# Kernel optimization log

Measured on AMD Instinct MI355X. Metric: run time of the kernel, lower is better.

Reference implementation:

```python
import jax, jax.numpy as jnp
import numpy as np

N = 100000
E = 1600000
IN_DIM = 20
HID = 32
HEADS = 4
OUT = 64
NEG_SLOPE = 0.2


def _p(key, shape, scale=0.1):
    return jax.random.normal(key, shape, dtype=jnp.float32) * scale


def setup_inputs() -> dict:
    key = jax.random.key(0)
    ks = jax.random.split(key, 20)
    x = jax.random.normal(ks[0], (N, IN_DIM), dtype=jnp.float32)
    edge_index = jax.random.randint(ks[1], (2, E), 0, N, dtype=jnp.int32)
    edge_attr = jax.random.uniform(ks[2], (E, 1), dtype=jnp.float32)
    HC1 = HEADS * HID
    return {
        "x": x,
        "edge_index": edge_index,
        "edge_attr": edge_attr,
        "Wl1": _p(ks[3], (HC1, IN_DIM)), "bl1": jnp.zeros((HC1,), jnp.float32),
        "Wr1": _p(ks[4], (HC1, IN_DIM)), "br1": jnp.zeros((HC1,), jnp.float32),
        "We1": _p(ks[5], (HC1, 1)),
        "att1": _p(ks[6], (HEADS, HID)),
        "b1": jnp.zeros((HC1,), jnp.float32),
        "Wl2": _p(ks[7], (OUT, HC1)), "bl2": jnp.zeros((OUT,), jnp.float32),
        "Wr2": _p(ks[8], (OUT, HC1)), "br2": jnp.zeros((OUT,), jnp.float32),
        "We2": _p(ks[9], (OUT, 1)),
        "att2": _p(ks[10], (1, OUT)),
        "b2": jnp.zeros((OUT,), jnp.float32),
    }


def gatv2_conv(x, src, dst, edge_attr, Wl, bl, Wr, br, We, att, bias, heads, ch, concat):
    n = x.shape[0]
    # add self loops; edge_attr fill_value = mean (PyG default)
    loop = jnp.arange(n, dtype=src.dtype)
    src = jnp.concatenate([src, loop])
    dst = jnp.concatenate([dst, loop])
    ea_fill = jnp.broadcast_to(edge_attr.mean(axis=0, keepdims=True), (n, edge_attr.shape[1]))
    edge_attr = jnp.concatenate([edge_attr, ea_fill], axis=0)

    xl = (x @ Wl.T + bl).reshape(n, heads, ch)   # source transform [N,H,C]
    xr = (x @ Wr.T + br).reshape(n, heads, ch)   # target transform [N,H,C]
    ee = (edge_attr @ We.T).reshape(-1, heads, ch)  # edge embed [E',H,C]

    e = xl[src] + xr[dst] + ee                    # [E',H,C]
    e = jax.nn.leaky_relu(e, NEG_SLOPE)
    logits = jnp.einsum('ehc,hc->eh', e, att)     # [E',H]

    # segment softmax over destination nodes (every node has a self loop)
    mx = jax.ops.segment_max(logits, dst, num_segments=n)
    ex = jnp.exp(logits - mx[dst])
    denom = jax.ops.segment_sum(ex, dst, num_segments=n)
    alpha = ex / denom[dst]                       # [E',H]

    msg = xl[src] * alpha[:, :, None]             # [E',H,C]
    out = jax.ops.segment_sum(msg, dst, num_segments=n)  # [N,H,C]
    out = out.reshape(n, heads * ch) if concat else out.mean(axis=1)
    return out + bias


def reference(x, edge_index, edge_attr, Wl1, bl1, Wr1, br1, We1, att1, b1,
              Wl2, bl2, Wr2, br2, We2, att2, b2):
    src, dst = edge_index[0], edge_index[1]
    h = gatv2_conv(x, src, dst, edge_attr, Wl1, bl1, Wr1, br1, We1, att1, b1,
                   HEADS, HID, concat=True)
    h = jax.nn.elu(h)  # dropout is identity in eval mode
    out = gatv2_conv(h, src, dst, edge_attr, Wl2, bl2, Wr2, br2, We2, att2, b2,
                     1, OUT, concat=False)
    return out
```

## Files before the change

### kernel.cpp

```cpp
#include <hip/hip_runtime.h>
#include <cstdint>
#include <cstddef>

#define NNODES 100000
#define NEDGES 1600000
#define IN_DIM 20
#define HID    32
#define HEADS  4
#define HC1    128
#define OUTC   64
#define NEG    0.2f
#define LOG2E  1.4426950408889634f
#define NCHUNK ((NNODES + 255) / 256)
#define NBLK   ((NNODES + 63) / 64)

typedef _Float16 h2 __attribute__((ext_vector_type(2)));
typedef __fp16   hh2 __attribute__((ext_vector_type(2)));
union U4H { uint4 u; h2 h[4]; };
union U2H { uint2 u; h2 h[2]; };

#if __has_builtin(__builtin_amdgcn_fdot2)
#define FDOT2(a, b, c) __builtin_amdgcn_fdot2(__builtin_bit_cast(hh2, (a)), __builtin_bit_cast(hh2, (b)), (c), false)
#else
#define FDOT2(a, b, c) ((c) + (float)(a).x * (float)(b).x + (float)(a).y * (float)(b).y)
#endif

__global__ void k_sum(const float* __restrict__ ea, int n, float* __restrict__ out) {
    float s = 0.0f;
    for (int i = blockIdx.x * blockDim.x + threadIdx.x; i < n; i += gridDim.x * blockDim.x)
        s += ea[i];
    #pragma unroll
    for (int off = 32; off > 0; off >>= 1) s += __shfl_down(s, off, 64);
    __shared__ float ls[4];
    int lane = threadIdx.x & 63, wid = threadIdx.x >> 6;
    if (lane == 0) ls[wid] = s;
    __syncthreads();
    if (threadIdx.x == 0) {
        float t = ls[0] + ls[1] + ls[2] + ls[3];
        atomicAdd(out, t);
    }
}

__global__ void k_hist(const int* __restrict__ ei, int* __restrict__ cnt,
                       int* __restrict__ erank) {
    int e = blockIdx.x * blockDim.x + threadIdx.x;
    if (e < NEDGES) erank[e] = atomicAdd(&cnt[ei[NEDGES + e]], 1);
}

__global__ void k_scan_chunk(const int* __restrict__ cnt, int* __restrict__ rowptr,
                             int* __restrict__ csums) {
    __shared__ int s[256];
    int i = blockIdx.x * 256 + threadIdx.x;
    int v = (i < NNODES) ? cnt[i] : 0;
    s[threadIdx.x] = v;
    __syncthreads();
    for (int off = 1; off < 256; off <<= 1) {
        int t = (threadIdx.x >= off) ? s[threadIdx.x - off] : 0;
        __syncthreads();
        s[threadIdx.x] += t;
        __syncthreads();
    }
    if (i < NNODES) rowptr[i] = s[threadIdx.x] - v;
    if (threadIdx.x == 255) csums[blockIdx.x] = s[255];
}

__global__ void k_scan_tops(int* __restrict__ csums) {
    __shared__ int s[512];
    int v = (threadIdx.x < NCHUNK) ? csums[threadIdx.x] : 0;
    s[threadIdx.x] = v;
    __syncthreads();
    for (int off = 1; off < 512; off <<= 1) {
        int t = (threadIdx.x >= off) ? s[threadIdx.x - off] : 0;
        __syncthreads();
        s[threadIdx.x] += t;
        __syncthreads();
    }
    if (threadIdx.x < NCHUNK) csums[threadIdx.x] = s[threadIdx.x] - v;
}

__global__ void k_scan_add(int* __restrict__ rowptr, const int* __restrict__ csums) {
    int i = blockIdx.x * 256 + threadIdx.x;
    if (i < NNODES) rowptr[i] += csums[blockIdx.x];
    if (i == 0) rowptr[NNODES] = NEDGES;
}

__global__ void k_scatter(const int* __restrict__ ei, const float* __restrict__ ea,
                          const int* __restrict__ rowptr, const int* __restrict__ erank,
                          int2* __restrict__ cedge) {
    int e = blockIdx.x * blockDim.x + threadIdx.x;
    if (e >= NEDGES) return;
    int dst = ei[NEDGES + e];
    int pos = rowptr[dst] + erank[e];
    cedge[pos] = make_int2(ei[e], __float_as_int(ea[e]));
}

__global__ void k_prep(const float* __restrict__ Wl1, const float* __restrict__ Wr1,
                       float* __restrict__ Bt1,
                       const float* __restrict__ Wl2, const float* __restrict__ Wr2,
                       float* __restrict__ Bt2,
                       const float* __restrict__ We1, const float* __restrict__ att1,
                       _Float16* __restrict__ Weh1, _Float16* __restrict__ Ath1,
                       const float* __restrict__ We2, const float* __restrict__ att2,
                       _Float16* __restrict__ Weh2, _Float16* __restrict__ Ath2) {
    int idx = blockIdx.x * 256 + threadIdx.x;
    if (idx < 16384) {
        int k = idx >> 7, c = idx & 127;
        Bt2[idx] = (c < 64) ? Wl2[c * HC1 + k] : Wr2[(c - 64) * HC1 + k];
    }
    int i1 = idx - 16384;
    if (i1 >= 0 && i1 < 5120) {
        int k = i1 >> 8, c = i1 & 255;
        Bt1[i1] = (c < 128) ? Wl1[c * IN_DIM + k] : Wr1[(c - 128) * IN_DIM + k];
    }
    int i2 = idx - (16384 + 5120);
    if (i2 >= 0 && i2 < 128) {
        Weh1[i2] = (_Float16)We1[i2];
        Ath1[i2] = (_Float16)(att1[i2] * LOG2E);
    }
    int i3 = idx - (16384 + 5120 + 128);
    if (i3 >= 0 && i3 < 64) {
        Weh2[i3] = (_Float16)We2[i3];
        Ath2[i3] = (_Float16)(att2[i3] * LOG2E);
    }
}

__global__ __launch_bounds__(256) void k_gemm1(
        const float* __restrict__ x, const float* __restrict__ Bt,
        const float* __restrict__ bl, const float* __restrict__ br,
        _Float16* __restrict__ xlh, _Float16* __restrict__ xrh) {
    __shared__ float sA[64 * IN_DIM];
    __shared__ float sB[IN_DIM * 256];
    int nb = blockIdx.x * 64;
    int tid = threadIdx.x;
    {
        size_t base = (size_t)nb * IN_DIM;
        size_t maxf = (size_t)NNODES * IN_DIM;
        for (int f = tid * 4; f < 64 * IN_DIM; f += 1024) {
            float4 v;
            if (base + f + 4 <= maxf) v = *(const float4*)(x + base + f);
            else                      v = *(const float4*)(x + maxf - 4);
            *(float4*)(sA + f) = v;
        }
    }
    for (int f = tid * 4; f < IN_DIM * 256; f += 1024)
        *(float4*)(sB + f) = *(const float4*)(Bt + f);
    __syncthreads();

    int tn = tid & 7, tc = tid >> 3;
    float acc[8][8];
    #pragma unroll
    for (int i = 0; i < 8; ++i)
        #pragma unroll
        for (int c = 0; c < 8; ++c) acc[i][c] = 0.0f;

    #pragma unroll
    for (int kt = 0; kt < 5; ++kt) {
        float4 a[8], b0[4], b1[4];
        #pragma unroll
        for (int i = 0; i < 8; ++i)
            a[i] = *(const float4*)(sA + (tn + 8 * i) * IN_DIM + kt * 4);
        #pragma unroll
        for (int j = 0; j < 4; ++j) {
            b0[j] = *(const float4*)(sB + (kt * 4 + j) * 256 + tc * 8);
            b1[j] = *(const float4*)(sB + (kt * 4 + j) * 256 + tc * 8 + 4);
        }
        #pragma unroll
        for (int i = 0; i < 8; ++i) {
            const float* ap = (const float*)&a[i];
            #pragma unroll
            for (int j = 0; j < 4; ++j) {
                float av = ap[j];
                const float* p0 = (const float*)&b0[j];
                const float* p1 = (const float*)&b1[j];
                #pragma unroll
                for (int c = 0; c < 4; ++c) {
                    acc[i][c]     += av * p0[c];
                    acc[i][c + 4] += av * p1[c];
                }
            }
        }
    }
    int c0 = tc * 8;
    float4 bias0, bias1;
    if (c0 < 128) {
        bias0 = *(const float4*)(bl + c0);
        bias1 = *(const float4*)(bl + c0 + 4);
    } else {
        bias0 = *(const float4*)(br + c0 - 128);
        bias1 = *(const float4*)(br + c0 - 124);
    }
    const float* q0 = (const float*)&bias0;
    const float* q1 = (const float*)&bias1;
    #pragma unroll
    for (int i = 0; i < 8; ++i) {
        int n = nb + tn + 8 * i;
        if (n >= NNODES) continue;
        float w[8];
        #pragma unroll
        for (int c = 0; c < 4; ++c) { w[c] = acc[i][c] + q0[c]; w[c + 4] = acc[i][c + 4] + q1[c]; }
        U4H ph;
        #pragma unroll
        for (int c = 0; c < 4; ++c) {
            h2 t; t.x = (_Float16)w[2 * c]; t.y = (_Float16)w[2 * c + 1];
            ph.h[c] = t;
        }
        if (c0 < 128) *(uint4*)(xlh + (size_t)n * HC1 + c0)       = ph.u;
        else          *(uint4*)(xrh + (size_t)n * HC1 + c0 - 128) = ph.u;
    }
}

__global__ __launch_bounds__(256) void k_gemm2(
        const _Float16* __restrict__ h1h, const float* __restrict__ Bt,
        const float* __restrict__ bl, const float* __restrict__ br,
        _Float16* __restrict__ xl2h, _Float16* __restrict__ xr2h) {
    __shared__ float sA[64 * 132];
    __shared__ float sB[32 * 128];
    int nb = blockIdx.x * 64;
    int tid = threadIdx.x;
    for (int idx = tid * 8; idx < 64 * HC1; idx += 2048) {
        int node = idx >> 7, k = idx & 127;
        int gn = nb + node; if (gn >= NNODES) gn = NNODES - 1;
        U4H v; v.u = *(const uint4*)(h1h + ((size_t)gn << 7) + k);
        float4 f0, f1;
        f0.x = (float)v.h[0].x; f0.y = (float)v.h[0].y;
        f0.z = (float)v.h[1].x; f0.w = (float)v.h[1].y;
        f1.x = (float)v.h[2].x; f1.y = (float)v.h[2].y;
        f1.z = (float)v.h[3].x; f1.w = (float)v.h[3].y;
        *(float4*)(sA + node * 132 + k)     = f0;
        *(float4*)(sA + node * 132 + k + 4) = f1;
    }
    int tn = tid & 7, tc = tid >> 3;
    float acc[8][4];
    #pragma unroll
    for (int i = 0; i < 8; ++i)
        #pragma unroll
        for (int c = 0; c < 4; ++c) acc[i][c] = 0.0f;

    for (int kc = 0; kc < 4; ++kc) {
        __syncthreads();
        for (int f = tid * 4; f < 32 * 128; f += 1024)
            *(float4*)(sB + f) = *(const float4*)(Bt + kc * 4096 + f);
        __syncthreads();
        #pragma unroll
        for (int ks = 0; ks < 8; ++ks) {
            int k0 = kc * 32 + ks * 4;
            float4 a[8], b[4];
            #pragma unroll
            for (int i = 0; i < 8; ++i)
                a[i] = *(const float4*)(sA + (tn + 8 * i) * 132 + k0);
            #pragma unroll
            for (int j = 0; j < 4; ++j)
                b[j] = *(const float4*)(sB + (ks * 4 + j) * 128 + tc * 4);
            #pragma unroll
            for (int i = 0; i < 8; ++i) {
                const float* ap = (const float*)&a[i];
                #pragma unroll
                for (int j = 0; j < 4; ++j) {
                    float av = ap[j];
                    const float* bp = (const float*)&b[j];
                    #pragma unroll
                    for (int c = 0; c < 4; ++c) acc[i][c] += av * bp[c];
                }
            }
        }
    }
    int c0 = tc * 4;
    float4 bias;
    if (c0 < 64) bias = *(const float4*)(bl + c0);
    else         bias = *(const float4*)(br + c0 - 64);
    const float* q = (const float*)&bias;
    #pragma unroll
    for (int i = 0; i < 8; ++i) {
        int n = nb + tn + 8 * i;
        if (n >= NNODES) continue;
        float w[4];
        #pragma unroll
        for (int c = 0; c < 4; ++c) w[c] = acc[i][c] + q[c];
        U2H ph;
        h2 t0; t0.x = (_Float16)w[0]; t0.y = (_Float16)w[1];
        h2 t1; t1.x = (_Float16)w[2]; t1.y = (_Float16)w[3];
        ph.h[0] = t0; ph.h[1] = t1;
        if (c0 < 64) *(uint2*)(xl2h + (size_t)n * OUTC + c0)      = ph.u;
        else         *(uint2*)(xr2h + (size_t)n * OUTC + c0 - 64) = ph.u;
    }
}

__global__ __launch_bounds__(256) void k_node1(
        const int* __restrict__ rowptr, const int2* __restrict__ cedge,
        const float* __restrict__ easum,
        const _Float16* __restrict__ xlh, const _Float16* __restrict__ xrh,
        const _Float16* __restrict__ Weh, const _Float16* __restrict__ Ath,
        const float* __restrict__ bias, _Float16* __restrict__ h1h) {
    int n = blockIdx.x * 4 + (threadIdx.x >> 6);
    if (n >= NNODES) return;
    int lane = threadIdx.x & 63;
    int g = lane >> 4;
    int q = lane & 15;
    int c = q * 8;
    U4H xru; xru.u = *(const uint4*)(xrh + ((unsigned)n << 7) + c);
    U4H weu; weu.u = *(const uint4*)(Weh + c);
    U4H atu; atu.u = *(const uint4*)(Ath + c);
    h2 neg2; neg2.x = (_Float16)NEG; neg2.y = neg2.x;
    h2 zero; zero.x = (_Float16)0; zero.y = zero.x;
    h2 acc2[4] = { zero, zero, zero, zero };
    float s = 0.0f;
    int start = rowptr[n], deg = rowptr[n + 1] - start;

    {
        U4H xss; xss.u = *(const uint4*)(xlh + ((unsigned)n << 7) + c);
        float amean = easum[0] * (1.0f / (float)NEDGES);
        h2 a2; a2.x = (_Float16)amean; a2.y = a2.x;
        float p = 0.0f;
        #pragma unroll
        for (int j = 0; j < 4; ++j) {
            h2 e = xss.h[j] + (a2 * weu.h[j] + xru.h[j]);
            h2 l = __builtin_elementwise_max(e, neg2 * e);
            p = FDOT2(l, atu.h[j], p);
        }
        p += __shfl_xor(p, 1, 64);
        p += __shfl_xor(p, 2, 64);
        if (g == 0) {
            float pe = exp2f(p);
            s += pe;
            h2 pe2; pe2.x = (_Float16)pe; pe2.y = pe2.x;
            #pragma unroll
            for (int j = 0; j < 4; ++j) acc2[j] += pe2 * xss.h[j];
        }
    }

    if (deg > 0) {
        int dm1 = deg - 1;
        int2 eca = cedge[start + (g < dm1 ? g : dm1)];
        int2 ecb = cedge[start + (4 + g < dm1 ? 4 + g : dm1)];
        int2 ena = cedge[start + (8 + g < dm1 ? 8 + g : dm1)];
        int2 enb = cedge[start + (12 + g < dm1 ? 12 + g : dm1)];
        U4H xa, xb;
        xa.u = *(const uint4*)(xlh + ((unsigned)eca.x << 7) + c);
        xb.u = *(const uint4*)(xlh + ((unsigned)ecb.x << 7) + c);
        for (int base = 0; base < deg; base += 8) {
            int2 cA = eca, cB = ecb;
            U4H xA = xa, xB = xb;
            if (base + 8 < deg) {
                xa.u = *(const uint4*)(xlh + ((unsigned)ena.x << 7) + c);
                xb.u = *(const uint4*)(xlh + ((unsigned)enb.x << 7) + c);
                eca = ena; ecb = enb;
                int oA = base + 16 + g, oB = base + 20 + g;
                ena = cedge[start + (oA < dm1 ? oA : dm1)];
                enb = cedge[start + (oB < dm1 ? oB : dm1)];
            }
            {
                h2 a2; a2.x = (_Float16)__int_as_float(cA.y); a2.y = a2.x;
                float p = 0.0f;
                #pragma unroll
                for (int j = 0; j < 4; ++j) {
                    h2 e = xA.h[j] + (a2 * weu.h[j] + xru.h[j]);
                    h2 l = __builtin_elementwise_max(e, neg2 * e);
                    p = FDOT2(l, atu.h[j], p);
                }
                p += __shfl_xor(p, 1, 64);
                p += __shfl_xor(p, 2, 64);
                float pe = (base + g < deg) ? exp2f(p) : 0.0f;
                s += pe;
                h2 pe2; pe2.x = (_Float16)pe; pe2.y = pe2.x;
                #pragma unroll
                for (int j = 0; j < 4; ++j) acc2[j] += pe2 * xA.h[j];
            }
            {
                h2 a2; a2.x = (_Float16)__int_as_float(cB.y); a2.y = a2.x;
                float p = 0.0f;
                #pragma unroll
                for (int j = 0; j < 4; ++j) {
                    h2 e = xB.h[j] + (a2 * weu.h[j] + xru.h[j]);
                    h2 l = __builtin_elementwise_max(e, neg2 * e);
                    p = FDOT2(l, atu.h[j], p);
                }
                p += __shfl_xor(p, 1, 64);
                p += __shfl_xor(p, 2, 64);
                float pe = (base + 4 + g < deg) ? exp2f(p) : 0.0f;
                s += pe;
                h2 pe2; pe2.x = (_Float16)pe; pe2.y = pe2.x;
                #pragma unroll
                for (int j = 0; j < 4; ++j) acc2[j] += pe2 * xB.h[j];
            }
        }
    }
    #pragma unroll
    for (int off = 16; off <= 32; off <<= 1) {
        s += __shfl_xor(s, off, 64);
        #pragma unroll
        for (int j = 0; j < 4; ++j) {
            int lv = __builtin_bit_cast(int, acc2[j]);
            int t = __shfl_xor(lv, off, 64);
            acc2[j] += __builtin_bit_cast(h2, t);
        }
    }
    if (g == 0) {
        float inv = 1.0f / s;
        float4 bi0 = *(const float4*)(bias + c), bi1 = *(const float4*)(bias + c + 4);
        const float* bq = (const float*)&bi0;
        const float* br_ = (const float*)&bi1;
        float o[8];
        #pragma unroll
        for (int j = 0; j < 4; ++j) {
            o[2 * j]     = (float)acc2[j].x * inv + (j < 2 ? bq[2 * j]     : br_[2 * j - 4]);
            o[2 * j + 1] = (float)acc2[j].y * inv + (j < 2 ? bq[2 * j + 1] : br_[2 * j - 3]);
        }
        #pragma unroll
        for (int k = 0; k < 8; ++k) o[k] = o[k] > 0.0f ? o[k] : expm1f(o[k]);
        U4H ph;
        #pragma unroll
        for (int k = 0; k < 4; ++k) {
            h2 t; t.x = (_Float16)o[2 * k]; t.y = (_Float16)o[2 * k + 1];
            ph.h[k] = t;
        }
        *(uint4*)(h1h + ((unsigned)n << 7) + c) = ph.u;
    }
}

__global__ __launch_bounds__(256) void k_node2(
        const int* __restrict__ rowptr, const int2* __restrict__ cedge,
        const float* __restrict__ easum,
        const _Float16* __restrict__ xl2h, const _Float16* __restrict__ xr2h,
        const _Float16* __restrict__ Weh, const _Float16* __restrict__ Ath,
        const float* __restrict__ bias, float* __restrict__ out) {
    int n = blockIdx.x * 4 + (threadIdx.x >> 6);
    if (n >= NNODES) return;
    int lane = threadIdx.x & 63;
    int g = lane >> 3;
    int q = lane & 7;
    int c = q * 8;
    U4H xru; xru.u = *(const uint4*)(xr2h + ((unsigned)n << 6) + c);
    U4H weu; weu.u = *(const uint4*)(Weh + c);
    U4H atu; atu.u = *(const uint4*)(Ath + c);
    h2 neg2; neg2.x = (_Float16)NEG; neg2.y = neg2.x;
    h2 zero; zero.x = (_Float16)0; zero.y = zero.x;
    h2 acc2[4] = { zero, zero, zero, zero };
    float s = 0.0f;
    int start = rowptr[n], deg = rowptr[n + 1] - start;

    {
        U4H xss; xss.u = *(const uint4*)(xl2h + ((unsigned)n << 6) + c);
        float amean = easum[0] * (1.0f / (float)NEDGES);
        h2 a2; a2.x = (_Float16)amean; a2.y = a2.x;
        float p = 0.0f;
        #pragma unroll
        for (int j = 0; j < 4; ++j) {
            h2 e = xss.h[j] + (a2 * weu.h[j] + xru.h[j]);
            h2 l = __builtin_elementwise_max(e, neg2 * e);
            p = FDOT2(l, atu.h[j], p);
        }
        p += __shfl_xor(p, 1, 64);
        p += __shfl_xor(p, 2, 64);
        p += __shfl_xor(p, 4, 64);
        if (g == 0) {
            float pe = exp2f(p);
            s += pe;
            h2 pe2; pe2.x = (_Float16)pe; pe2.y = pe2.x;
            #pragma unroll
            for (int j = 0; j < 4; ++j) acc2[j] += pe2 * xss.h[j];
        }
    }

    if (deg > 0) {
        int dm1 = deg - 1;
        int2 ec = cedge[start + (g < dm1 ? g : dm1)];
        int2 en = cedge[start + (8 + g < dm1 ? 8 + g : dm1)];
        U4H xs;
        xs.u = *(const uint4*)(xl2h + ((unsigned)ec.x << 6) + c);
        for (int base = 0; base < deg; base += 8) {
            int2 cE = ec;
            U4H xC = xs;
            if (base + 8 < deg) {
                xs.u = *(const uint4*)(xl2h + ((unsigned)en.x << 6) + c);
                ec = en;
                int o = base + 16 + g;
                en = cedge[start + (o < dm1 ? o : dm1)];
            }
            h2 a2; a2.x = (_Float16)__int_as_float(cE.y); a2.y = a2.x;
            float p = 0.0f;
            #pragma unroll
            for (int j = 0; j < 4; ++j) {
                h2 e = xC.h[j] + (a2 * weu.h[j] + xru.h[j]);
                h2 l = __builtin_elementwise_max(e, neg2 * e);
                p = FDOT2(l, atu.h[j], p);
            }
            p += __shfl_xor(p, 1, 64);
            p += __shfl_xor(p, 2, 64);
            p += __shfl_xor(p, 4, 64);
            float pe = (base + g < deg) ? exp2f(p) : 0.0f;
            s += pe;
            h2 pe2; pe2.x = (_Float16)pe; pe2.y = pe2.x;
            #pragma unroll
            for (int j = 0; j < 4; ++j) acc2[j] += pe2 * xC.h[j];
        }
    }
    #pragma unroll
    for (int off = 8; off <= 32; off <<= 1) {
        s += __shfl_xor(s, off, 64);
        #pragma unroll
        for (int j = 0; j < 4; ++j) {
            int lv = __builtin_bit_cast(int, acc2[j]);
            int t = __shfl_xor(lv, off, 64);
            acc2[j] += __builtin_bit_cast(h2, t);
        }
    }
    if (g == 0) {
        float inv = 1.0f / s;
        float4 bi0 = *(const float4*)(bias + c), bi1 = *(const float4*)(bias + c + 4);
        const float* bq0 = (const float*)&bi0;
        const float* bq1 = (const float*)&bi1;
        float4 o0, o1;
        o0.x = (float)acc2[0].x * inv + bq0[0];  o0.y = (float)acc2[0].y * inv + bq0[1];
        o0.z = (float)acc2[1].x * inv + bq0[2];  o0.w = (float)acc2[1].y * inv + bq0[3];
        o1.x = (float)acc2[2].x * inv + bq1[0];  o1.y = (float)acc2[2].y * inv + bq1[1];
        o1.z = (float)acc2[3].x * inv + bq1[2];  o1.w = (float)acc2[3].y * inv + bq1[3];
        float4* op = (float4*)(out + (size_t)n * OUTC + c);
        op[0] = o0; op[1] = o1;
    }
}

extern "C" void kernel_launch(void* const* d_in, const int* in_sizes, int n_in,
                              void* d_out, int out_size, void* d_ws, size_t ws_size,
                              hipStream_t stream) {
    (void)in_sizes; (void)n_in; (void)out_size; (void)ws_size;
    const float* x    = (const float*)d_in[0];
    const int*   ei   = (const int*)d_in[1];
    const float* ea   = (const float*)d_in[2];
    const float* Wl1  = (const float*)d_in[3];
    const float* bl1  = (const float*)d_in[4];
    const float* Wr1  = (const float*)d_in[5];
    const float* br1  = (const float*)d_in[6];
    const float* We1  = (const float*)d_in[7];
    const float* att1 = (const float*)d_in[8];
    const float* b1   = (const float*)d_in[9];
    const float* Wl2  = (const float*)d_in[10];
    const float* bl2  = (const float*)d_in[11];
    const float* Wr2  = (const float*)d_in[12];
    const float* br2  = (const float*)d_in[13];
    const float* We2  = (const float*)d_in[14];
    const float* att2 = (const float*)d_in[15];
    const float* b2   = (const float*)d_in[16];
    float* out = (float*)d_out;

    char* wsb = (char*)d_ws;
    _Float16* xlh  = (_Float16*)wsb; wsb += (size_t)NNODES * HC1 * 2;
    _Float16* xrh  = (_Float16*)wsb; wsb += (size_t)NNODES * HC1 * 2;
    _Float16* h1h  = (_Float16*)wsb; wsb += (size_t)NNODES * HC1 * 2;
    int2*   cedge  = (int2*)wsb;     wsb += (size_t)NEDGES * 8;
    int*    erank  = (int*)wsb;      wsb += (size_t)NEDGES * 4;
    int*    cnt    = (int*)wsb;      wsb += (size_t)NNODES * 4;
    int*    rowptr = (int*)wsb;      wsb += ((size_t)(NNODES + 4) * 4);
    int*    csums  = (int*)wsb;      wsb += 512 * 4;
    float*  easum  = (float*)wsb;    wsb += 16;
    float*  Bt1    = (float*)wsb;    wsb += 20 * 256 * 4;
    float*  Bt2    = (float*)wsb;    wsb += 128 * 128 * 4;
    _Float16* Weh1 = (_Float16*)wsb; wsb += 128 * 2;
    _Float16* Ath1 = (_Float16*)wsb; wsb += 128 * 2;
    _Float16* Weh2 = (_Float16*)wsb; wsb += 64 * 2;
    _Float16* Ath2 = (_Float16*)wsb; wsb += 64 * 2;
    _Float16* xl2h = xlh;
    _Float16* xr2h = xrh;

    hipMemsetAsync(easum, 0, sizeof(float), stream);
    hipMemsetAsync(cnt, 0, (size_t)NNODES * 4, stream);

    k_sum<<<256, 256, 0, stream>>>(ea, NEDGES, easum);
    k_hist<<<(NEDGES + 255) / 256, 256, 0, stream>>>(ei, cnt, erank);
    k_prep<<<(16384 + 5120 + 128 + 64 + 255) / 256, 256, 0, stream>>>(
        Wl1, Wr1, Bt1, Wl2, Wr2, Bt2, We1, att1, Weh1, Ath1, We2, att2, Weh2, Ath2);
    k_scan_chunk<<<NCHUNK, 256, 0, stream>>>(cnt, rowptr, csums);
    k_scan_tops<<<1, 512, 0, stream>>>(csums);
    k_scan_add<<<NCHUNK, 256, 0, stream>>>(rowptr, csums);
    k_scatter<<<(NEDGES + 255) / 256, 256, 0, stream>>>(ei, ea, rowptr, erank, cedge);

    k_gemm1<<<NBLK, 256, 0, stream>>>(x, Bt1, bl1, br1, xlh, xrh);
    k_node1<<<(NNODES + 3) / 4, 256, 0, stream>>>(rowptr, cedge, easum,
                                                  xlh, xrh, Weh1, Ath1, b1, h1h);

    k_gemm2<<<NBLK, 256, 0, stream>>>(h1h, Bt2, bl2, br2, xl2h, xr2h);
    k_node2<<<(NNODES + 3) / 4, 256, 0, stream>>>(rowptr, cedge, easum,
                                                  xl2h, xr2h, Weh2, Ath2, b2, out);
}
```

Baseline: 449.9 us.

## Sort nodes by degree for load balance and shorten gather prefetch pipeline

Adds a counting sort of nodes by in-degree, capped at 63, using three small kernels that build a permutation. k_node1 and k_node2 then process nodes in that order, so waves within a block get similar degrees and lanes idle less. The node kernels also drop the deep software prefetch of source-feature rows: they now prefetch only the next edge descriptors and load the features just in time. This lowers register pressure, but more gather latency is exposed, degree-sorted order loses output locality, and three extra launches are added.

```diff
diff --git a/kernel.cpp b/kernel.cpp
--- a/kernel.cpp
+++ b/kernel.cpp
@@ -92,6 +92,34 @@
     int dst = ei[NEDGES + e];
     int pos = rowptr[dst] + erank[e];
     cedge[pos] = make_int2(ei[e], __float_as_int(ea[e]));
+}
+
+__global__ void k_dhist(const int* __restrict__ rowptr, int* __restrict__ bcnt,
+                        int* __restrict__ nrank) {
+    int n = blockIdx.x * 256 + threadIdx.x;
+    if (n >= NNODES) return;
+    int d = rowptr[n + 1] - rowptr[n];
+    if (d > 63) d = 63;
+    nrank[n] = atomicAdd(&bcnt[d], 1);
+}
+__global__ void k_dscan(const int* __restrict__ bcnt, int* __restrict__ bbase) {
+    int lane = threadIdx.x;
+    int v = bcnt[lane];
+    int sum = v;
+    #pragma unroll
+    for (int off = 1; off < 64; off <<= 1) {
+        int t = __shfl_up(sum, off, 64);
+        if (lane >= off) sum += t;
+    }
+    bbase[lane] = sum - v;
+}
+__global__ void k_place(const int* __restrict__ rowptr, const int* __restrict__ nrank,
+                        const int* __restrict__ bbase, int* __restrict__ perm) {
+    int n = blockIdx.x * 256 + threadIdx.x;
+    if (n >= NNODES) return;
+    int d = rowptr[n + 1] - rowptr[n];
+    if (d > 63) d = 63;
+    perm[bbase[d] + nrank[n]] = n;
 }
 
 __global__ void k_prep(const float* __restrict__ Wl1, const float* __restrict__ Wr1,
@@ -286,13 +314,15 @@
 }
 
 __global__ __launch_bounds__(256) void k_node1(
+        const int* __restrict__ perm,
         const int* __restrict__ rowptr, const int2* __restrict__ cedge,
         const float* __restrict__ easum,
         const _Float16* __restrict__ xlh, const _Float16* __restrict__ xrh,
         const _Float16* __restrict__ Weh, const _Float16* __restrict__ Ath,
         const float* __restrict__ bias, _Float16* __restrict__ h1h) {
-    int n = blockIdx.x * 4 + (threadIdx.x >> 6);
-    if (n >= NNODES) return;
+    int slot = blockIdx.x * 4 + (threadIdx.x >> 6);
+    if (slot >= NNODES) return;
+    int n = perm[slot];
     int lane = threadIdx.x & 63;
     int g = lane >> 4;
     int q = lane & 15;
@@ -330,24 +360,18 @@
 
     if (deg > 0) {
         int dm1 = deg - 1;
-        int2 eca = cedge[start + (g < dm1 ? g : dm1)];
-        int2 ecb = cedge[start + (4 + g < dm1 ? 4 + g : dm1)];
-        int2 ena = cedge[start + (8 + g < dm1 ? 8 + g : dm1)];
-        int2 enb = cedge[start + (12 + g < dm1 ? 12 + g : dm1)];
-        U4H xa, xb;
-        xa.u = *(const uint4*)(xlh + ((unsigned)eca.x << 7) + c);
-        xb.u = *(const uint4*)(xlh + ((unsigned)ecb.x << 7) + c);
+        int2 epA = cedge[start + (g < dm1 ? g : dm1)];
+        int2 epB = cedge[start + (4 + g < dm1 ? 4 + g : dm1)];
         for (int base = 0; base < deg; base += 8) {
-            int2 cA = eca, cB = ecb;
-            U4H xA = xa, xB = xb;
-            if (base + 8 < deg) {
-                xa.u = *(const uint4*)(xlh + ((unsigned)ena.x << 7) + c);
-                xb.u = *(const uint4*)(xlh + ((unsigned)enb.x << 7) + c);
-                eca = ena; ecb = enb;
-                int oA = base + 16 + g, oB = base + 20 + g;
-                ena = cedge[start + (oA < dm1 ? oA : dm1)];
-                enb = cedge[start + (oB < dm1 ? oB : dm1)];
+            int2 cA = epA, cB = epB;
+            int nxt = base + 8;
+            if (nxt < deg) {
+                int oA = nxt + g, oB = nxt + 4 + g;
+                epA = cedge[start + (oA < dm1 ? oA : dm1)];
+                epB = cedge[start + (oB < dm1 ? oB : dm1)];
             }
+            U4H xA; xA.u = *(const uint4*)(xlh + ((unsigned)cA.x << 7) + c);
+            U4H xB; xB.u = *(const uint4*)(xlh + ((unsigned)cB.x << 7) + c);
             {
                 h2 a2; a2.x = (_Float16)__int_as_float(cA.y); a2.y = a2.x;
                 float p = 0.0f;
@@ -418,13 +442,15 @@
 }
 
 __global__ __launch_bounds__(256) void k_node2(
+        const int* __restrict__ perm,
         const int* __restrict__ rowptr, const int2* __restrict__ cedge,
         const float* __restrict__ easum,
         const _Float16* __restrict__ xl2h, const _Float16* __restrict__ xr2h,
         const _Float16* __restrict__ Weh, const _Float16* __restrict__ Ath,
         const float* __restrict__ bias, float* __restrict__ out) {
-    int n = blockIdx.x * 4 + (threadIdx.x >> 6);
-    if (n >= NNODES) return;
+    int slot = blockIdx.x * 4 + (threadIdx.x >> 6);
+    if (slot >= NNODES) return;
+    int n = perm[slot];
     int lane = threadIdx.x & 63;
     int g = lane >> 3;
     int q = lane & 7;
@@ -463,19 +489,15 @@
 
     if (deg > 0) {
         int dm1 = deg - 1;
-        int2 ec = cedge[start + (g < dm1 ? g : dm1)];
-        int2 en = cedge[start + (8 + g < dm1 ? 8 + g : dm1)];
-        U4H xs;
-        xs.u = *(const uint4*)(xl2h + ((unsigned)ec.x << 6) + c);
+        int2 ep = cedge[start + (g < dm1 ? g : dm1)];
         for (int base = 0; base < deg; base += 8) {
-            int2 cE = ec;
-            U4H xC = xs;
-            if (base + 8 < deg) {
-                xs.u = *(const uint4*)(xl2h + ((unsigned)en.x << 6) + c);
-                ec = en;
-                int o = base + 16 + g;
-                en = cedge[start + (o < dm1 ? o : dm1)];
+            int2 cE = ep;
+            int nxt = base + 8;
+            if (nxt < deg) {
+                int o = nxt + g;
+                ep = cedge[start + (o < dm1 ? o : dm1)];
             }
+            U4H xC; xC.u = *(const uint4*)(xl2h + ((unsigned)cE.x << 6) + c);
             h2 a2; a2.x = (_Float16)__int_as_float(cE.y); a2.y = a2.x;
             float p = 0.0f;
             #pragma unroll
@@ -550,7 +572,10 @@
     int*    erank  = (int*)wsb;      wsb += (size_t)NEDGES * 4;
     int*    cnt    = (int*)wsb;      wsb += (size_t)NNODES * 4;
     int*    rowptr = (int*)wsb;      wsb += ((size_t)(NNODES + 4) * 4);
+    int*    perm   = (int*)wsb;      wsb += (size_t)NNODES * 4;
     int*    csums  = (int*)wsb;      wsb += 512 * 4;
+    int*    bcnt   = (int*)wsb;      wsb += 64 * 4;
+    int*    bbase  = (int*)wsb;      wsb += 64 * 4;
     float*  easum  = (float*)wsb;    wsb += 16;
     float*  Bt1    = (float*)wsb;    wsb += 20 * 256 * 4;
     float*  Bt2    = (float*)wsb;    wsb += 128 * 128 * 4;
@@ -560,9 +585,11 @@
     _Float16* Ath2 = (_Float16*)wsb; wsb += 64 * 2;
     _Float16* xl2h = xlh;
     _Float16* xr2h = xrh;
+    int* nrank = cnt;
 
     hipMemsetAsync(easum, 0, sizeof(float), stream);
     hipMemsetAsync(cnt, 0, (size_t)NNODES * 4, stream);
+    hipMemsetAsync(bcnt, 0, 64 * 4, stream);
 
     k_sum<<<256, 256, 0, stream>>>(ea, NEDGES, easum);
     k_hist<<<(NEDGES + 255) / 256, 256, 0, stream>>>(ei, cnt, erank);
@@ -573,11 +600,15 @@
     k_scan_add<<<NCHUNK, 256, 0, stream>>>(rowptr, csums);
     k_scatter<<<(NEDGES + 255) / 256, 256, 0, stream>>>(ei, ea, rowptr, erank, cedge);
 
+    k_dhist<<<NCHUNK, 256, 0, stream>>>(rowptr, bcnt, nrank);
+    k_dscan<<<1, 64, 0, stream>>>(bcnt, bbase);
+    k_place<<<NCHUNK, 256, 0, stream>>>(rowptr, nrank, bbase, perm);
+
     k_gemm1<<<NBLK, 256, 0, stream>>>(x, Bt1, bl1, br1, xlh, xrh);
-    k_node1<<<(NNODES + 3) / 4, 256, 0, stream>>>(rowptr, cedge, easum,
+    k_node1<<<(NNODES + 3) / 4, 256, 0, stream>>>(perm, rowptr, cedge, easum,
                                                   xlh, xrh, Weh1, Ath1, b1, h1h);
 
     k_gemm2<<<NBLK, 256, 0, stream>>>(h1h, Bt2, bl2, br2, xl2h, xr2h);
-    k_node2<<<(NNODES + 3) / 4, 256, 0, stream>>>(rowptr, cedge, easum,
+    k_node2<<<(NNODES + 3) / 4, 256, 0, stream>>>(perm, rowptr, cedge, easum,
                                                   xl2h, xr2h, Weh2, Ath2, b2, out);
 }
```

Result: slower. 743.5 us (+65.3%).
